# Kernel tuning notes

Hardware: AMD Instinct MI355X
Metric: run time of the kernel (lower is better)

## Reference

```python
import jax, jax.numpy as jnp
import numpy as np

D_EMB_IN = 1024
D_K = 64
D_EMB_OUT = 1024
NB_HEADS = 16


def setup_inputs() -> dict:
    key = jax.random.key(0)
    k1, k2, k3, k4, k5 = jax.random.split(key, 5)
    scale = 0.02
    X = jax.random.normal(k1, (2, 2048, D_EMB_IN), dtype=jnp.float32)
    # nn.Linear weights are [out, in]; we store them transposed-ready as [in, out]
    Wq = jax.random.normal(k2, (D_EMB_IN, NB_HEADS * D_K), dtype=jnp.float32) * scale
    Wk = jax.random.normal(k3, (D_EMB_IN, NB_HEADS * D_K), dtype=jnp.float32) * scale
    Wv = jax.random.normal(k4, (D_EMB_IN, NB_HEADS * D_K), dtype=jnp.float32) * scale
    Wo = jax.random.normal(k5, (NB_HEADS * D_K, D_EMB_OUT), dtype=jnp.float32) * scale
    return {"X": X, "Wq": Wq, "Wk": Wk, "Wv": Wv, "Wo": Wo}


def reference(X, Wq, Wk, Wv, Wo):
    B, T, _ = X.shape
    H, Dk = NB_HEADS, D_K
    # project and split heads: [B, H, T, Dk]
    def proj(W):
        return (X @ W).reshape(B, T, H, Dk).transpose(0, 2, 1, 3)
    Q, K, V = proj(Wq), proj(Wk), proj(Wv)
    S = jnp.einsum("bhqd,bhkd->bhqk", Q, K) / jnp.sqrt(jnp.float32(Dk))
    causal = jnp.tril(jnp.ones((T, T), dtype=bool))  # True = keep
    S = jnp.where(causal, S, -jnp.inf)
    P = jax.nn.softmax(S, axis=-1)
    A = jnp.einsum("bhqk,bhkd->bhqd", P, V)
    A = A.transpose(0, 2, 1, 3).reshape(B, T, H * Dk)
    return A @ Wo
```

## Files before the change

### kernel.cpp

```cpp
#include <hip/hip_runtime.h>
#include <hip/hip_bf16.h>


typedef unsigned short u16;
typedef __bf16 bf16x8 __attribute__((ext_vector_type(8)));
typedef float f32x4 __attribute__((ext_vector_type(4)));

#define TS 72
#define PS 136
#define NEG_INF (-1e30f)
#define SC_LOG2 0.1803368801f

#if __has_builtin(__builtin_amdgcn_exp2f)
#define EXP2(x) __builtin_amdgcn_exp2f(x)
#else
#define EXP2(x) exp2f(x)
#endif

#define GLD_LDS16(gp, lp) __builtin_amdgcn_global_load_lds( \
    (const __attribute__((address_space(1))) void*)(gp),    \
    (__attribute__((address_space(3))) void*)(lp), 16, 0, 0)

__device__ __forceinline__ bf16x8 as_bf16x8(int4 v) { return __builtin_bit_cast(bf16x8, v); }
__device__ __forceinline__ u16 bf16_bits(float f) { return __builtin_bit_cast(u16, (__bf16)f); }

__device__ __forceinline__ bool detect_f32(const void* X) {
    const u16* x16 = (const u16*)X;
    int lane = threadIdx.x & 63;
    int hits = 0;
#pragma unroll
    for (int i = 0; i < 4; ++i) {
        u16 v = x16[lane * 4 + i];
        hits += (((v >> 7) & 0xFF) > 130) ? 1 : 0;
    }
    return __popcll(__ballot(hits > 0)) >= 8;
}

__device__ __forceinline__ bf16x8 load8(const void* p, size_t eoff, bool f32m) {
    if (!f32m) return as_bf16x8(*(const int4*)((const u16*)p + eoff));
    const float* f = (const float*)p + eoff;
    float4 a = *(const float4*)f;
    float4 b = *(const float4*)(f + 4);
    bf16x8 r;
    r[0] = (__bf16)a.x; r[1] = (__bf16)a.y; r[2] = (__bf16)a.z; r[3] = (__bf16)a.w;
    r[4] = (__bf16)b.x; r[5] = (__bf16)b.y; r[6] = (__bf16)b.z; r[7] = (__bf16)b.w;
    return r;
}

__global__ __launch_bounds__(256) void prep_all(const void* __restrict__ Wq,
                                                const void* __restrict__ Wk,
                                                const void* __restrict__ Wv,
                                                const void* __restrict__ Wo,
                                                const void* __restrict__ X,
                                                u16* __restrict__ Wt3,
                                                u16* __restrict__ Wot,
                                                u16* __restrict__ Xbf) {
    bool f32m = detect_f32(X);
    int z = blockIdx.z;
    if (z == 4) {
        int blk = blockIdx.y * 16 + blockIdx.x;
        size_t base = (size_t)blk * 16384 + threadIdx.x * 8;
#pragma unroll
        for (int i = 0; i < 8; ++i) {
            size_t eoff = base + (size_t)i * 2048;
            bf16x8 v = load8(X, eoff, f32m);
            *(int4*)(Xbf + eoff) = __builtin_bit_cast(int4, v);
        }
        return;
    }
    const void* in = (z == 0) ? Wq : (z == 1) ? Wk : (z == 2) ? Wv : Wo;
    u16* out = (z < 3) ? (Wt3 + (size_t)z * (1u << 20)) : Wot;
    __shared__ alignas(16) u16 T[64][TS];
    int r0 = blockIdx.y * 64, c0 = blockIdx.x * 64;
    int tr = threadIdx.x >> 3, tc8 = threadIdx.x & 7;
    bf16x8 v0 = load8(in, (size_t)(r0 + tr) * 1024 + c0 + tc8 * 8, f32m);
    bf16x8 v1 = load8(in, (size_t)(r0 + tr + 32) * 1024 + c0 + tc8 * 8, f32m);
    *(int4*)&T[tr][tc8 * 8]      = __builtin_bit_cast(int4, v0);
    *(int4*)&T[tr + 32][tc8 * 8] = __builtin_bit_cast(int4, v1);
    __syncthreads();
    for (int half = 0; half < 2; ++half) {
        int cr = tr + half * 32;
        u16 tmp[8];
#pragma unroll
        for (int i = 0; i < 8; ++i) tmp[i] = T[tc8 * 8 + i][cr];
        *(int4*)(out + (size_t)(c0 + cr) * 1024 + r0 + tc8 * 8) = *(int4*)tmp;
    }
}

__global__ __launch_bounds__(256, 4) void gemm128(const u16* __restrict__ A,
                                                  const u16* __restrict__ Bt,
                                                  u16* __restrict__ Cq, u16* __restrict__ Ck,
                                                  u16* __restrict__ Cv) {
    __shared__ alignas(16) u16 As[128 * 64];
    __shared__ alignas(16) u16 Bs[128 * 64];
    const int K = 1024;
    int tid = threadIdx.x, wave = tid >> 6, lane = tid & 63;
    int quad = lane >> 4, l16 = lane & 15;
    int wrow = wave >> 1, wcol = wave & 1;
    int m0 = blockIdx.x * 128, n0 = blockIdx.y * 128;
    int rlane = lane >> 3, kc = lane & 7;
    int scol = (kc ^ rlane) * 8;

    f32x4 acc[4][4] = {};

    for (int k0 = 0; k0 < K; k0 += 64) {
        __syncthreads();
#pragma unroll
        for (int i = 0; i < 4; ++i) {
            int rc = wave * 4 + i;
            GLD_LDS16(A  + (size_t)(m0 + rc * 8 + rlane) * K + k0 + scol, As + rc * 512);
            GLD_LDS16(Bt + (size_t)(n0 + rc * 8 + rlane) * K + k0 + scol, Bs + rc * 512);
        }
        __syncthreads();
#pragma unroll
        for (int ks = 0; ks < 2; ++ks) {
            bf16x8 af[4], bfr[4];
#pragma unroll
            for (int i = 0; i < 4; ++i) {
                int row = wrow * 64 + i * 16 + l16;
                af[i] = as_bf16x8(*(const int4*)(As + row * 64 + (((ks * 4 + quad) ^ (row & 7)) * 8)));
            }
#pragma unroll
            for (int j = 0; j < 4; ++j) {
                int row = wcol * 64 + j * 16 + l16;
                bfr[j] = as_bf16x8(*(const int4*)(Bs + row * 64 + (((ks * 4 + quad) ^ (row & 7)) * 8)));
            }
#pragma unroll
            for (int i = 0; i < 4; ++i)
#pragma unroll
                for (int j = 0; j < 4; ++j)
                    acc[i][j] = __builtin_amdgcn_mfma_f32_16x16x32_bf16(af[i], bfr[j], acc[i][j], 0, 0, 0);
        }
    }

#pragma unroll
    for (int i = 0; i < 4; ++i)
#pragma unroll
        for (int j = 0; j < 4; ++j)
#pragma unroll
            for (int r = 0; r < 4; ++r) {
                int m = m0 + wrow * 64 + i * 16 + quad * 4 + r;
                int n = n0 + wcol * 64 + j * 16 + l16;
                float f = acc[i][j][r];
                if (n < 1024)       Cq[(size_t)m * 1024 + n] = bf16_bits(f);
                else if (n < 2048)  Ck[(size_t)m * 1024 + n - 1024] = bf16_bits(f);
                else {
                    int n2 = n - 2048;
                    int bh = ((m >> 11) << 4) | (n2 >> 6), d = n2 & 63, t = m & 2047;
                    Cv[(((size_t)bh * 64 + d) << 11) + t] = bf16_bits(f);
                }
            }
}

__global__ __launch_bounds__(256, 4) void gemm_out(const u16* __restrict__ A,
                                                   const u16* __restrict__ Bt,
                                                   void* __restrict__ Cout,
                                                   const void* __restrict__ Xdet) {
    bool f32m = detect_f32(Xdet);
    __shared__ alignas(16) u16 As[64 * 64];
    __shared__ alignas(16) u16 Bs[128 * 64];
    const int K = 1024;
    int tid = threadIdx.x, wave = tid >> 6, lane = tid & 63;
    int quad = lane >> 4, l16 = lane & 15;
    int wrow = wave & 1, wcol = wave >> 1;
    int m0 = blockIdx.x * 64, n0 = blockIdx.y * 128;
    int rlane = lane >> 3, kc = lane & 7;
    int scol = (kc ^ rlane) * 8;

    f32x4 acc[2][4] = {};

    for (int k0 = 0; k0 < K; k0 += 64) {
        __syncthreads();
#pragma unroll
        for (int i = 0; i < 4; ++i) {
            int rc = wave * 4 + i;
            GLD_LDS16(Bt + (size_t)(n0 + rc * 8 + rlane) * K + k0 + scol, Bs + rc * 512);
        }
#pragma unroll
        for (int i = 0; i < 2; ++i) {
            int rc = wave * 2 + i;
            GLD_LDS16(A + (size_t)(m0 + rc * 8 + rlane) * K + k0 + scol, As + rc * 512);
        }
        __syncthreads();
#pragma unroll
        for (int ks = 0; ks < 2; ++ks) {
            bf16x8 af[2], bfr[4];
#pragma unroll
            for (int i = 0; i < 2; ++i) {
                int row = wrow * 32 + i * 16 + l16;
                af[i] = as_bf16x8(*(const int4*)(As + row * 64 + (((ks * 4 + quad) ^ (row & 7)) * 8)));
            }
#pragma unroll
            for (int j = 0; j < 4; ++j) {
                int row = wcol * 64 + j * 16 + l16;
                bfr[j] = as_bf16x8(*(const int4*)(Bs + row * 64 + (((ks * 4 + quad) ^ (row & 7)) * 8)));
            }
#pragma unroll
            for (int i = 0; i < 2; ++i)
#pragma unroll
                for (int j = 0; j < 4; ++j)
                    acc[i][j] = __builtin_amdgcn_mfma_f32_16x16x32_bf16(af[i], bfr[j], acc[i][j], 0, 0, 0);
        }
    }

#pragma unroll
    for (int i = 0; i < 2; ++i)
#pragma unroll
        for (int j = 0; j < 4; ++j)
#pragma unroll
            for (int r = 0; r < 4; ++r) {
                int m = m0 + wrow * 32 + i * 16 + quad * 4 + r;
                int n = n0 + wcol * 64 + j * 16 + l16;
                float f = acc[i][j][r];
                if (f32m) ((float*)Cout)[(size_t)m * 1024 + n] = f;
                else      ((u16*)Cout)[(size_t)m * 1024 + n] = bf16_bits(f);
            }
}

__global__ __launch_bounds__(512, 4) void attn_kernel(const u16* __restrict__ Qb,
                                                      const u16* __restrict__ Kb,
                                                      const u16* __restrict__ Vt,
                                                      u16* __restrict__ Ab) {
    __shared__ alignas(16) u16 Ks[128 * 64];
    __shared__ alignas(16) u16 Vs[64 * 128];
    __shared__ alignas(16) u16 Ps[128 * PS];

    int tid = threadIdx.x, wave = tid >> 6, lane = tid & 63;
    int quad = lane >> 4, l16 = lane & 15;
    int bh = blockIdx.x;
    int J = 15 - blockIdx.y;
    int b = bh >> 4, h = bh & 15;
    int q0 = J * 128;
    int kr4 = lane >> 3, kc = lane & 7;
    int vr4 = lane >> 4, vc = lane & 15;

    const u16* qrow = Qb + (size_t)(b * 2048 + q0 + wave * 16 + l16) * 1024 + h * 64;
    bf16x8 qa0 = as_bf16x8(*(const int4*)(qrow + quad * 8));
    bf16x8 qa1 = as_bf16x8(*(const int4*)(qrow + 32 + quad * 8));

    f32x4 o[4] = {};
    float lrow[4] = {0.0f, 0.0f, 0.0f, 0.0f};

    const u16* kbase = Kb + (size_t)(b * 2048) * 1024 + h * 64;
    const u16* vbase = Vt + (size_t)bh * 64 * 2048;

    for (int j2 = 0; j2 <= J; ++j2) {
        int t0 = j2 * 128;
        __syncthreads();
#pragma unroll
        for (int i = 0; i < 2; ++i) {
            int rb = (wave * 2 + i) * 8;
            int grow = rb + kr4;
            int gch = kc ^ (grow & 7);
            GLD_LDS16(kbase + (size_t)(t0 + grow) * 1024 + gch * 8, Ks + rb * 64);
        }
#pragma unroll
        for (int i = 0; i < 2; ++i) {
            int rb = (wave * 2 + i) * 4;
            int grow = rb + vr4;
            int gch = vc ^ (grow & 15);
            GLD_LDS16(vbase + (size_t)grow * 2048 + t0 + gch * 8, Vs + rb * 128);
        }
        __syncthreads();

        bool diag = (j2 == J);
        int ntc = diag ? ((wave & ~1) + 2) : 8;

        f32x4 s[8];
#pragma unroll
        for (int nt = 0; nt < 8; ++nt) {
            if (nt >= ntc) continue;
            if (diag && nt > wave) {
                s[nt][0] = NEG_INF; s[nt][1] = NEG_INF; s[nt][2] = NEG_INF; s[nt][3] = NEG_INF;
                continue;
            }
            int row = nt * 16 + l16;
            int sw = row & 7;
            f32x4 a = {};
            bf16x8 b0 = as_bf16x8(*(const int4*)(Ks + row * 64 + ((quad ^ sw) * 8)));
            a = __builtin_amdgcn_mfma_f32_16x16x32_bf16(qa0, b0, a, 0, 0, 0);
            bf16x8 b1 = as_bf16x8(*(const int4*)(Ks + row * 64 + (((4 + quad) ^ sw) * 8)));
            a = __builtin_amdgcn_mfma_f32_16x16x32_bf16(qa1, b1, a, 0, 0, 0);
            a = a * SC_LOG2;
            if (diag && nt == wave) {
#pragma unroll
                for (int r = 0; r < 4; ++r)
                    if (l16 > quad * 4 + r) a[r] = NEG_INF;
            }
            s[nt] = a;
        }

#pragma unroll
        for (int r = 0; r < 4; ++r) {
            float psum = 0.0f;
            int prow = (wave * 16 + quad * 4 + r) * PS;
#pragma unroll
            for (int nt = 0; nt < 8; ++nt) {
                if (nt >= ntc) continue;
                float p = EXP2(s[nt][r]);
                psum += p;
                Ps[prow + nt * 16 + l16] = bf16_bits(p);
            }
            psum += __shfl_xor(psum, 1, 16);
            psum += __shfl_xor(psum, 2, 16);
            psum += __shfl_xor(psum, 4, 16);
            psum += __shfl_xor(psum, 8, 16);
            lrow[r] += psum;
        }

        int ksm = ntc >> 1;
#pragma unroll
        for (int ks = 0; ks < 4; ++ks) {
            if (ks >= ksm) continue;
            bf16x8 pa = as_bf16x8(*(const int4*)(Ps + (wave * 16 + l16) * PS + ks * 32 + quad * 8));
#pragma unroll
            for (int d4 = 0; d4 < 4; ++d4) {
                int vrow = d4 * 16 + l16;
                bf16x8 vb = as_bf16x8(*(const int4*)(Vs + vrow * 128 + (((ks * 4 + quad) ^ l16) * 8)));
                o[d4] = __builtin_amdgcn_mfma_f32_16x16x32_bf16(pa, vb, o[d4], 0, 0, 0);
            }
        }
    }

    u16* arow = Ab + (size_t)(b * 2048 + q0 + wave * 16) * 1024 + h * 64;
#pragma unroll
    for (int r = 0; r < 4; ++r) {
        float inv = 1.0f / lrow[r];
#pragma unroll
        for (int d4 = 0; d4 < 4; ++d4)
            arow[(quad * 4 + r) * 1024 + d4 * 16 + l16] = bf16_bits(o[d4][r] * inv);
    }
}

extern "C" void kernel_launch(void* const* d_in, const int* in_sizes, int n_in,
                              void* d_out, int out_size, void* d_ws, size_t ws_size,
                              hipStream_t stream) {
    (void)in_sizes; (void)n_in; (void)out_size; (void)ws_size;
    const void* X  = d_in[0];
    const void* Wq = d_in[1];
    const void* Wk = d_in[2];
    const void* Wv = d_in[3];
    const void* Wo = d_in[4];
    u16* ws16 = (u16*)d_ws;
    const size_t M1 = 1u << 20;
    u16* Xbf = ws16 + 0 * M1;
    u16* Wt3 = ws16 + 4 * M1;
    u16* Qb  = ws16 + 7 * M1;
    u16* Kb  = ws16 + 11 * M1;
    u16* Vt  = ws16 + 15 * M1;
    u16* Wot = ws16 + 19 * M1;
    u16* Ab  = ws16 + 0 * M1;

    prep_all<<<dim3(16, 16, 5), 256, 0, stream>>>(Wq, Wk, Wv, Wo, X, Wt3, Wot, Xbf);
    gemm128<<<dim3(32, 24), 256, 0, stream>>>(Xbf, Wt3, Qb, Kb, Vt);
    attn_kernel<<<dim3(32, 16), 512, 0, stream>>>(Qb, Kb, Vt, Ab);
    gemm_out<<<dim3(64, 8), 256, 0, stream>>>(Ab, Wot, d_out, X);
}
```

Baseline: 180.5 us.

## Double-buffer 64-key K/V tiles with async LDS prefetch and balanced block order

Splits each 128-key step into two 64-key tiles and double-buffers K and V in LDS. The next tile's global-to-LDS loads are issued right after compute, and explicit vmcnt waits replace the two full syncthreads per iteration, so load latency is meant to overlap with MFMA and softmax work. The P staging buffer shrinks and the V swizzle changes to match the 64-wide tile. Blocks on grid.y are also interleaved (long then short query tiles) to balance causal work across CUs. This brings more barriers per key and relies on hand-placed waitcnt and barrier ordering for correctness.

```diff
diff --git a/kernel.cpp b/kernel.cpp
--- a/kernel.cpp
+++ b/kernel.cpp
@@ -7,7 +7,7 @@
 typedef float f32x4 __attribute__((ext_vector_type(4)));
 
 #define TS 72
-#define PS 136
+#define PS2 72
 #define NEG_INF (-1e30f)
 #define SC_LOG2 0.1803368801f
 
@@ -20,6 +20,11 @@
 #define GLD_LDS16(gp, lp) __builtin_amdgcn_global_load_lds( \
     (const __attribute__((address_space(1))) void*)(gp),    \
     (__attribute__((address_space(3))) void*)(lp), 16, 0, 0)
+
+#define WAITV2() asm volatile("s_waitcnt vmcnt(2)" ::: "memory")
+#define WAITV0() asm volatile("s_waitcnt vmcnt(0)" ::: "memory")
+#define SBAR()   __builtin_amdgcn_s_barrier()
+#define SCHED0() __builtin_amdgcn_sched_barrier(0)
 
 __device__ __forceinline__ bf16x8 as_bf16x8(int4 v) { return __builtin_bit_cast(bf16x8, v); }
 __device__ __forceinline__ u16 bf16_bits(float f) { return __builtin_bit_cast(u16, (__bf16)f); }
@@ -221,18 +226,19 @@
                                                       const u16* __restrict__ Kb,
                                                       const u16* __restrict__ Vt,
                                                       u16* __restrict__ Ab) {
-    __shared__ alignas(16) u16 Ks[128 * 64];
-    __shared__ alignas(16) u16 Vs[64 * 128];
-    __shared__ alignas(16) u16 Ps[128 * PS];
+    __shared__ alignas(16) u16 Ks[2][64 * 64];
+    __shared__ alignas(16) u16 Vs[2][64 * 64];
+    __shared__ alignas(16) u16 Ps[128 * PS2];
 
     int tid = threadIdx.x, wave = tid >> 6, lane = tid & 63;
     int quad = lane >> 4, l16 = lane & 15;
     int bh = blockIdx.x;
-    int J = 15 - blockIdx.y;
+    int J = (blockIdx.y < 8) ? (15 - (int)blockIdx.y) : ((int)blockIdx.y - 8);
     int b = bh >> 4, h = bh & 15;
     int q0 = J * 128;
-    int kr4 = lane >> 3, kc = lane & 7;
-    int vr4 = lane >> 4, vc = lane & 15;
+    int r8 = lane >> 3, kc = lane & 7;
+    int srow = wave * 8 + r8;
+    int sch = kc ^ (srow & 7);
 
     const u16* qrow = Qb + (size_t)(b * 2048 + q0 + wave * 16 + l16) * 1024 + h * 64;
     bf16x8 qa0 = as_bf16x8(*(const int4*)(qrow + quad * 8));
@@ -243,46 +249,45 @@
 
     const u16* kbase = Kb + (size_t)(b * 2048) * 1024 + h * 64;
     const u16* vbase = Vt + (size_t)bh * 64 * 2048;
-
-    for (int j2 = 0; j2 <= J; ++j2) {
-        int t0 = j2 * 128;
-        __syncthreads();
-#pragma unroll
-        for (int i = 0; i < 2; ++i) {
-            int rb = (wave * 2 + i) * 8;
-            int grow = rb + kr4;
-            int gch = kc ^ (grow & 7);
-            GLD_LDS16(kbase + (size_t)(t0 + grow) * 1024 + gch * 8, Ks + rb * 64);
-        }
-#pragma unroll
-        for (int i = 0; i < 2; ++i) {
-            int rb = (wave * 2 + i) * 4;
-            int grow = rb + vr4;
-            int gch = vc ^ (grow & 15);
-            GLD_LDS16(vbase + (size_t)grow * 2048 + t0 + gch * 8, Vs + rb * 128);
-        }
-        __syncthreads();
-
-        bool diag = (j2 == J);
-        int ntc = diag ? ((wave & ~1) + 2) : 8;
-
-        f32x4 s[8];
-#pragma unroll
-        for (int nt = 0; nt < 8; ++nt) {
+    const u16* ksrc = kbase + (size_t)srow * 1024 + sch * 8;
+    const u16* vsrc = vbase + (size_t)srow * 2048 + sch * 8;
+
+    const int NT = 2 * J + 2;
+
+    GLD_LDS16(ksrc, &Ks[0][wave * 512]);
+    GLD_LDS16(vsrc, &Vs[0][wave * 512]);
+    GLD_LDS16(ksrc + (size_t)64 * 1024, &Ks[1][wave * 512]);
+    GLD_LDS16(vsrc + 64, &Vs[1][wave * 512]);
+
+    for (int j2 = 0; j2 < NT; ++j2) {
+        int cur = j2 & 1;
+        const u16* KsC = Ks[cur];
+        const u16* VsC = Vs[cur];
+        if (j2 + 1 < NT) { WAITV2(); } else { WAITV0(); }
+        SCHED0();
+        SBAR();
+        SCHED0();
+
+        int lim = 8 * J + wave - 4 * j2;
+        int ntc = (lim >= 3) ? 4 : ((lim < 0) ? 0 : ((lim + 2) & ~1));
+
+        f32x4 s[4];
+#pragma unroll
+        for (int nt = 0; nt < 4; ++nt) {
             if (nt >= ntc) continue;
-            if (diag && nt > wave) {
+            if (nt > lim) {
                 s[nt][0] = NEG_INF; s[nt][1] = NEG_INF; s[nt][2] = NEG_INF; s[nt][3] = NEG_INF;
                 continue;
             }
             int row = nt * 16 + l16;
             int sw = row & 7;
             f32x4 a = {};
-            bf16x8 b0 = as_bf16x8(*(const int4*)(Ks + row * 64 + ((quad ^ sw) * 8)));
+            bf16x8 b0 = as_bf16x8(*(const int4*)(KsC + row * 64 + ((quad ^ sw) * 8)));
             a = __builtin_amdgcn_mfma_f32_16x16x32_bf16(qa0, b0, a, 0, 0, 0);
-            bf16x8 b1 = as_bf16x8(*(const int4*)(Ks + row * 64 + (((4 + quad) ^ sw) * 8)));
+            bf16x8 b1 = as_bf16x8(*(const int4*)(KsC + row * 64 + (((4 + quad) ^ sw) * 8)));
             a = __builtin_amdgcn_mfma_f32_16x16x32_bf16(qa1, b1, a, 0, 0, 0);
             a = a * SC_LOG2;
-            if (diag && nt == wave) {
+            if (nt == lim) {
 #pragma unroll
                 for (int r = 0; r < 4; ++r)
                     if (l16 > quad * 4 + r) a[r] = NEG_INF;
@@ -293,9 +298,9 @@
 #pragma unroll
         for (int r = 0; r < 4; ++r) {
             float psum = 0.0f;
-            int prow = (wave * 16 + quad * 4 + r) * PS;
-#pragma unroll
-            for (int nt = 0; nt < 8; ++nt) {
+            int prow = (wave * 16 + quad * 4 + r) * PS2;
+#pragma unroll
+            for (int nt = 0; nt < 4; ++nt) {
                 if (nt >= ntc) continue;
                 float p = EXP2(s[nt][r]);
                 psum += p;
@@ -310,15 +315,24 @@
 
         int ksm = ntc >> 1;
 #pragma unroll
-        for (int ks = 0; ks < 4; ++ks) {
+        for (int ks = 0; ks < 2; ++ks) {
             if (ks >= ksm) continue;
-            bf16x8 pa = as_bf16x8(*(const int4*)(Ps + (wave * 16 + l16) * PS + ks * 32 + quad * 8));
+            bf16x8 pa = as_bf16x8(*(const int4*)(Ps + (wave * 16 + l16) * PS2 + ks * 32 + quad * 8));
 #pragma unroll
             for (int d4 = 0; d4 < 4; ++d4) {
                 int vrow = d4 * 16 + l16;
-                bf16x8 vb = as_bf16x8(*(const int4*)(Vs + vrow * 128 + (((ks * 4 + quad) ^ l16) * 8)));
+                bf16x8 vb = as_bf16x8(*(const int4*)(VsC + vrow * 64 + (((ks * 4 + quad) ^ (vrow & 7)) * 8)));
                 o[d4] = __builtin_amdgcn_mfma_f32_16x16x32_bf16(pa, vb, o[d4], 0, 0, 0);
             }
+        }
+
+        SCHED0();
+        SBAR();
+        SCHED0();
+        if (j2 + 2 < NT) {
+            int t0n = (j2 + 2) * 64;
+            GLD_LDS16(ksrc + (size_t)t0n * 1024, &Ks[cur][wave * 512]);
+            GLD_LDS16(vsrc + t0n, &Vs[cur][wave * 512]);
         }
     }
 
```

Measured after the change: 202.0 us. 11.9% more time.
